# Kernel optimization log

Hardware: AMD Instinct MI355X
Metric: run time of the kernel (lower is better)

Reference implementation:

```python
import jax, jax.numpy as jnp
import numpy as np

N = 100000
E = 1600000
NEG_SLOPE = 0.2


def _param(key, shape, scale=0.05):
    return jax.random.normal(key, shape, dtype=jnp.float32) * scale


def setup_inputs() -> dict:
    key = jax.random.key(0)
    ks = jax.random.split(key, 16)
    x = jax.random.normal(ks[0], (N, 128), dtype=jnp.float32)
    edge_index = jax.random.randint(ks[1], (2, E), 0, N, dtype=jnp.int64)
    # layer 1: 128 -> (H=2, C=64), concat
    W1 = _param(ks[2], (128, 2 * 64)); a_src1 = _param(ks[3], (2, 64)); a_dst1 = _param(ks[4], (2, 64)); b1 = jnp.zeros((128,), jnp.float32)
    # layer 2: 128 -> (H=2, C=64), concat
    W2 = _param(ks[5], (128, 2 * 64)); a_src2 = _param(ks[6], (2, 64)); a_dst2 = _param(ks[7], (2, 64)); b2 = jnp.zeros((128,), jnp.float32)
    # layer 3: 128 -> (H=1, C=64), mean (concat=False)
    W3 = _param(ks[8], (128, 1 * 64)); a_src3 = _param(ks[9], (1, 64)); a_dst3 = _param(ks[10], (1, 64)); b3 = jnp.zeros((64,), jnp.float32)
    return {"x": x, "edge_index": edge_index,
            "W1": W1, "a_src1": a_src1, "a_dst1": a_dst1, "b1": b1,
            "W2": W2, "a_src2": a_src2, "a_dst2": a_dst2, "b2": b2,
            "W3": W3, "a_src3": a_src3, "a_dst3": a_dst3, "b3": b3}


def gat_layer(x, src, dst, W, a_src, a_dst, b, concat):
    H, C = a_src.shape
    n = x.shape[0]
    h = (x @ W).reshape(n, H, C)                      # [N,H,C]
    # per-node attention logits (avoid [E,H,C] gather for the score step)
    al_s = jnp.sum(h * a_src[None], axis=-1)          # [N,H]
    al_d = jnp.sum(h * a_dst[None], axis=-1)          # [N,H]
    e = al_s[src] + al_d[dst]                         # [E',H]
    e = jnp.where(e > 0, e, NEG_SLOPE * e)            # LeakyReLU(0.2)
    # scatter-softmax over incoming edges per destination node
    m = jax.ops.segment_max(e, dst, num_segments=n)   # [N,H]
    ex = jnp.exp(e - m[dst])
    z = jax.ops.segment_sum(ex, dst, num_segments=n)  # [N,H]
    alpha = ex / z[dst]                               # [E',H]
    msg = h[src] * alpha[:, :, None]                  # [E',H,C]
    out = jax.ops.segment_sum(msg, dst, num_segments=n)  # [N,H,C]
    out = out.reshape(n, H * C) if concat else out.mean(axis=1)
    return out + b


def reference(x, edge_index, W1, a_src1, a_dst1, b1, W2, a_src2, a_dst2, b2, W3, a_src3, a_dst3, b3):
    n = x.shape[0]
    loop = jnp.arange(n, dtype=edge_index.dtype)
    src = jnp.concatenate([edge_index[0], loop])      # add self-loops (PyG default)
    dst = jnp.concatenate([edge_index[1], loop])
    h = gat_layer(x, src, dst, W1, a_src1, a_dst1, b1, True)
    h = jax.nn.relu(h)
    h = gat_layer(h, src, dst, W2, a_src2, a_dst2, b2, True)
    h = jax.nn.relu(h)
    return gat_layer(h, src, dst, W3, a_src3, a_dst3, b3, False)
```

## Files before the change

kernel.cpp:

```cpp
#include <hip/hip_runtime.h>
#include <hip/hip_bf16.h>

#define NEG_SLOPE 0.2f
#define BUK_SHIFT 9
#define BUK_SIZE 512
#define BUK_CAP 16384

typedef unsigned short u16;
typedef __attribute__((ext_vector_type(4))) float f4v;
typedef _Float16 h8 __attribute__((ext_vector_type(8)));

__device__ __forceinline__ u16 f2h_bits(_Float16 h) {
    union { _Float16 f; u16 u; } c;
    c.f = h;
    return c.u;
}


__global__ void k_zero(int* g_cnt, int nb) {
    int i = blockIdx.x * blockDim.x + threadIdx.x;
    if (i < nb) g_cnt[i] = 0;
}

__launch_bounds__(256)
__global__ void k_binscatter(const int* __restrict__ ei, int* g_cnt, int* buckets,
                             int E, int nb) {
    __shared__ int lcnt[256], lbase[256], lcur[256];
    int t = threadIdx.x;
    if (t < nb) {
        lcnt[t] = 0;
        lcur[t] = 0;
    }
    __syncthreads();
    int tile0 = blockIdx.x * 4096;
    int pk[16], bk[16];
#pragma unroll
    for (int k = 0; k < 16; k++) {
        int idx = tile0 + k * 256 + t;
        bk[k] = -1;
        if (idx < E) {
            int s = ei[idx];
            int d = ei[E + idx];
            bk[k] = d >> BUK_SHIFT;
            pk[k] = (s << BUK_SHIFT) | (d & (BUK_SIZE - 1));
            atomicAdd(&lcnt[bk[k]], 1);
        }
    }
    __syncthreads();
    if (t < nb && lcnt[t] > 0) lbase[t] = atomicAdd(&g_cnt[t], lcnt[t]);
    __syncthreads();
#pragma unroll
    for (int k = 0; k < 16; k++) {
        if (bk[k] >= 0) {
            int p = lbase[bk[k]] + atomicAdd(&lcur[bk[k]], 1);
            if (p < BUK_CAP) buckets[(bk[k] << 14) + p] = pk[k];
        }
    }
}

__launch_bounds__(512)
__global__ void k_csr(const int* __restrict__ g_cnt, const int* __restrict__ buckets,
                      int* csr_ptr, int* csr_src, int n, int nb) {
    __shared__ int lcnt[512], lsc[512], lcur[512], bsc[512];
    int b = blockIdx.x;
    int t = threadIdx.x;
    int nodes = min(BUK_SIZE, n - b * BUK_SIZE);
    int cnt = min(g_cnt[b], BUK_CAP);
    const int* bp = &buckets[b << 14];

    int bv = 0;
    if (t < nb) bv = min(g_cnt[t], BUK_CAP) + min(BUK_SIZE, n - t * BUK_SIZE);
    bsc[t] = bv;
    __syncthreads();
    for (int off = 1; off < 512; off <<= 1) {
        int x = (t >= off) ? bsc[t - off] : 0;
        __syncthreads();
        bsc[t] += x;
        __syncthreads();
    }
    int boff = bsc[b] - (cnt + nodes);
    int total = bsc[nb - 1];
    __syncthreads();

    lcnt[t] = 0;
    __syncthreads();
    for (int i = t; i < cnt; i += 512) atomicAdd(&lcnt[bp[i] & (BUK_SIZE - 1)], 1);
    __syncthreads();
    int myc = (t < nodes) ? (lcnt[t] + 1) : 0;
    lsc[t] = myc;
    __syncthreads();
    for (int off = 1; off < 512; off <<= 1) {
        int x = (t >= off) ? lsc[t - off] : 0;
        __syncthreads();
        lsc[t] += x;
        __syncthreads();
    }
    int excl = lsc[t] - myc;
    lcur[t] = excl;
    if (t < nodes) csr_ptr[b * BUK_SIZE + t] = boff + excl;
    if (b == nb - 1 && t == 0) csr_ptr[n] = total;
    __syncthreads();
    for (int i = t; i < cnt; i += 512) {
        int v = bp[i];
        int ld = v & (BUK_SIZE - 1);
        int p = atomicAdd(&lcur[ld], 1);
        csr_src[boff + p] = v >> BUK_SHIFT;
    }
    if (t < nodes) {
        int p = atomicAdd(&lcur[t], 1);
        csr_src[boff + p] = b * BUK_SIZE + t;
    }
}


__global__ void k_wsplit_all(const float* __restrict__ W1, const float* __restrict__ W2,
                             const float* __restrict__ W3, u16* __restrict__ T1h,
                             u16* __restrict__ T1l, u16* __restrict__ T2h,
                             u16* __restrict__ T2l, u16* __restrict__ T3h,
                             u16* __restrict__ T3l) {
    int t = blockIdx.x * 256 + threadIdx.x;
    const float* W;
    u16 *Th, *Tl;
    int M, idx;
    if (t < 16384) {
        W = W1; Th = T1h; Tl = T1l; M = 128; idx = t;
    } else if (t < 32768) {
        W = W2; Th = T2h; Tl = T2l; M = 128; idx = t - 16384;
    } else if (t < 40960) {
        W = W3; Th = T3h; Tl = T3l; M = 64; idx = t - 32768;
    } else {
        return;
    }
    int c = idx >> 7, k = idx & 127;
    float v = W[(size_t)k * M + c];
    _Float16 h = (_Float16)v;
    _Float16 l = (_Float16)(v - (float)h);
    int ct = c >> 4, ch = k >> 5, q = (k >> 3) & 3, j = k & 7;
    size_t addr = ((size_t)ct * 4 + ch) * 512 + ((c & 15) + 16 * q) * 8 + j;
    Th[addr] = f2h_bits(h);
    Tl[addr] = f2h_bits(l);
}


__device__ __forceinline__ void load_split_f32(const float* __restrict__ X, int row,
                                               int koff, int N, h8& hi, h8& lo) {
    float v[8];
    if (row < N) {
        float4 a = *(const float4*)&X[(size_t)row * 128 + koff];
        float4 b = *(const float4*)&X[(size_t)row * 128 + koff + 4];
        v[0] = a.x; v[1] = a.y; v[2] = a.z; v[3] = a.w;
        v[4] = b.x; v[5] = b.y; v[6] = b.z; v[7] = b.w;
    } else {
#pragma unroll
        for (int i = 0; i < 8; i++) v[i] = 0.f;
    }
    union { h8 s; _Float16 u[8]; } H, L;
#pragma unroll
    for (int i = 0; i < 8; i++) {
        H.u[i] = (_Float16)v[i];
        L.u[i] = (_Float16)(v[i] - (float)H.u[i]);
    }
    hi = H.s;
    lo = L.s;
}

template <int M, bool FP32X>
__launch_bounds__(256)
__global__ void k_gemm_mfma(const float* __restrict__ Xf, const u16* __restrict__ XH,
                            const u16* __restrict__ WTh, const u16* __restrict__ WTl,
                            const float* __restrict__ asrc, const float* __restrict__ adst,
                            _Float16* __restrict__ Hout, float* __restrict__ als,
                            float* __restrict__ ald, int nrows) {
    const int CT = M / 16;
    const int H = (M == 128) ? 2 : 1;
    int tid = threadIdx.x;
    int wv = tid >> 6, lane = tid & 63;
    int q = lane >> 4, nl = lane & 15;
    int R0 = blockIdx.x * 128 + wv * 32;
    int rt0 = R0 >> 4;

    f4v acc[2][CT];
    f4v z4 = {0.f, 0.f, 0.f, 0.f};
#pragma unroll
    for (int rt = 0; rt < 2; rt++)
#pragma unroll
        for (int ct = 0; ct < CT; ct++) acc[rt][ct] = z4;

#pragma unroll
    for (int ch = 0; ch < 4; ch++) {
        h8 ah0, al0, ah1, al1;
        if (FP32X) {
            int koff = ch * 32 + q * 8;
            load_split_f32(Xf, R0 + nl, koff, nrows, ah0, al0);
            load_split_f32(Xf, R0 + 16 + nl, koff, nrows, ah1, al1);
        } else {
            size_t a0 = ((size_t)rt0 * 4 + ch) * 512 + lane * 8;
            size_t a1 = ((size_t)(rt0 + 1) * 4 + ch) * 512 + lane * 8;
            ah0 = *(const h8*)&XH[a0];
            ah1 = *(const h8*)&XH[a1];
        }
#pragma unroll
        for (int ct = 0; ct < CT; ct++) {
            size_t bb = ((size_t)ct * 4 + ch) * 512 + lane * 8;
            h8 bh = *(const h8*)&WTh[bb];
            h8 bl = *(const h8*)&WTl[bb];
            acc[0][ct] = __builtin_amdgcn_mfma_f32_16x16x32_f16(ah0, bh, acc[0][ct], 0, 0, 0);
            acc[0][ct] = __builtin_amdgcn_mfma_f32_16x16x32_f16(ah0, bl, acc[0][ct], 0, 0, 0);
            acc[1][ct] = __builtin_amdgcn_mfma_f32_16x16x32_f16(ah1, bh, acc[1][ct], 0, 0, 0);
            acc[1][ct] = __builtin_amdgcn_mfma_f32_16x16x32_f16(ah1, bl, acc[1][ct], 0, 0, 0);
            if (FP32X) {
                acc[0][ct] = __builtin_amdgcn_mfma_f32_16x16x32_f16(al0, bh, acc[0][ct], 0, 0, 0);
                acc[1][ct] = __builtin_amdgcn_mfma_f32_16x16x32_f16(al1, bh, acc[1][ct], 0, 0, 0);
            }
        }
    }

    float av[CT], dvv[CT];
#pragma unroll
    for (int ct = 0; ct < CT; ct++) {
        av[ct] = asrc[ct * 16 + nl];
        dvv[ct] = adst[ct * 16 + nl];
    }
    float ps[2][4][2], pd[2][4][2];
#pragma unroll
    for (int rt = 0; rt < 2; rt++)
#pragma unroll
        for (int r = 0; r < 4; r++)
            for (int h = 0; h < 2; h++) ps[rt][r][h] = pd[rt][r][h] = 0.f;
#pragma unroll
    for (int rt = 0; rt < 2; rt++)
#pragma unroll
        for (int ct = 0; ct < CT; ct++) {
            int h = (M == 128) ? (ct >> 2) : 0;
#pragma unroll
            for (int r = 0; r < 4; r++) {
                ps[rt][r][h] = fmaf(acc[rt][ct][r], av[ct], ps[rt][r][h]);
                pd[rt][r][h] = fmaf(acc[rt][ct][r], dvv[ct], pd[rt][r][h]);
            }
        }

#pragma unroll
    for (int rt = 0; rt < 2; rt++)
#pragma unroll
        for (int ct = 0; ct < CT; ct++)
#pragma unroll
            for (int r = 0; r < 4; r++) {
                int row = R0 + rt * 16 + q * 4 + r;
                if (row < nrows) Hout[(size_t)row * M + ct * 16 + nl] = (_Float16)acc[rt][ct][r];
            }

#pragma unroll
    for (int rt = 0; rt < 2; rt++)
#pragma unroll
        for (int r = 0; r < 4; r++)
#pragma unroll
            for (int h = 0; h < H; h++) {
                float v1 = ps[rt][r][h], v2 = pd[rt][r][h];
                for (int m = 1; m <= 8; m <<= 1) {
                    v1 += __shfl_xor(v1, m);
                    v2 += __shfl_xor(v2, m);
                }
                int row = R0 + rt * 16 + q * 4 + r;
                if (nl == 0 && row < nrows) {
                    als[(size_t)row * H + h] = v1;
                    ald[(size_t)row * H + h] = v2;
                }
            }
}


__launch_bounds__(256)
__global__ void k_agg128(const int* __restrict__ ptr, const int* __restrict__ srcv,
                         const _Float16* __restrict__ Hh, const float* __restrict__ als,
                         const float* __restrict__ ald, const float* __restrict__ bias,
                         u16* __restrict__ OutX, int n) {
    int wid = (blockIdx.x * blockDim.x + threadIdx.x) >> 6;
    int lane = threadIdx.x & 63;
    if (wid >= n) return;
    int start = ptr[wid], end = ptr[wid + 1];
    float2 adv = *(const float2*)&ald[(size_t)wid * 2];
    int grp = lane >> 4;
    int gl = lane & 15;
    int hsel = gl >> 3;
    float z0 = 0.f, z1 = 0.f;
    float acc[8];
#pragma unroll
    for (int c = 0; c < 8; c++) acc[c] = 0.f;

    for (int base = start; base < end; base += 64) {
        int i = base + lane;
        int s_l = 0;
        float ex0 = 0.f, ex1 = 0.f;
        if (i < end) {
            s_l = srcv[i];
            float2 av = *(const float2*)&als[(size_t)s_l * 2];
            float e0 = av.x + adv.x;
            e0 = e0 > 0.f ? e0 : NEG_SLOPE * e0;
            ex0 = __expf(e0);
            float e1 = av.y + adv.y;
            e1 = e1 > 0.f ? e1 : NEG_SLOPE * e1;
            ex1 = __expf(e1);
        }
        z0 += ex0;
        z1 += ex1;
        int cntj = min(64, end - base);
        for (int jp = 0; jp < cntj; jp += 32) {
            int nk = min(8, (cntj - jp + 3) >> 2);
            h8 hv[8];
            float w[8];
#pragma unroll
            for (int k = 0; k < 8; k++) {
                if (k < nk) {
                    int j = jp + 4 * k + grp;
                    int s = __shfl(s_l, j);
                    float w0 = __shfl(ex0, j);
                    float w1 = __shfl(ex1, j);
                    w[k] = hsel ? w1 : w0;
                    hv[k] = *(const h8*)&Hh[(size_t)s * 128 + gl * 8];
                }
            }
#pragma unroll
            for (int k = 0; k < 8; k++) {
                if (k < nk) {
#pragma unroll
                    for (int c = 0; c < 8; c++)
                        acc[c] = fmaf(w[k], (float)hv[k][c], acc[c]);
                }
            }
        }
    }

#pragma unroll
    for (int c = 0; c < 8; c++) {
        acc[c] += __shfl_xor(acc[c], 16);
        acc[c] += __shfl_xor(acc[c], 32);
    }
    for (int m = 32; m >= 1; m >>= 1) {
        z0 += __shfl_xor(z0, m);
        z1 += __shfl_xor(z1, m);
    }
    if (lane < 16) {
        float zinv = hsel ? (1.f / z1) : (1.f / z0);
        int c0 = gl * 8;
        float4 b0 = *(const float4*)&bias[c0];
        float4 b1 = *(const float4*)&bias[c0 + 4];
        float bb[8] = {b0.x, b0.y, b0.z, b0.w, b1.x, b1.y, b1.z, b1.w};
        union { _Float16 f[8]; h8 v; } O;
#pragma unroll
        for (int c = 0; c < 8; c++) {
            float o = fmaxf(fmaf(acc[c], zinv, bb[c]), 0.f);
            O.f[c] = (_Float16)o;
        }
        int ch = c0 >> 5, qq = (c0 >> 3) & 3;
        size_t tb = ((size_t)(wid >> 4) * 4 + ch) * 512 + ((size_t)((wid & 15) + 16 * qq)) * 8;
        *(h8*)&OutX[tb] = O.v;
    }
}


__launch_bounds__(256)
__global__ void k_agg64(const int* __restrict__ ptr, const int* __restrict__ srcv,
                        const _Float16* __restrict__ Hh, const float* __restrict__ als,
                        const float* __restrict__ ald, const float* __restrict__ bias,
                        float* __restrict__ Out, int n) {
    int wid = blockIdx.x * 4 + (threadIdx.x >> 6);
    int lane = threadIdx.x & 63;
    if (wid >= n) return;
    int start = ptr[wid], end = ptr[wid + 1];
    float ad0 = ald[wid];
    int grp = lane >> 3;
    int gl = lane & 7;
    float z = 0.f;
    float acc[8];
#pragma unroll
    for (int c = 0; c < 8; c++) acc[c] = 0.f;

    for (int base = start; base < end; base += 64) {
        int i = base + lane;
        int s_l = 0;
        float ex0 = 0.f;
        if (i < end) {
            s_l = srcv[i];
            float e = als[s_l] + ad0;
            e = e > 0.f ? e : NEG_SLOPE * e;
            ex0 = __expf(e);
        }
        z += ex0;
        int cntj = min(64, end - base);
        int nk = (cntj + 7) >> 3;
        h8 hv[8];
        float w[8];
#pragma unroll
        for (int k = 0; k < 8; k++) {
            if (k < nk) {
                int j = 8 * k + grp;
                int s = __shfl(s_l, j);
                w[k] = __shfl(ex0, j);
                hv[k] = *(const h8*)&Hh[(size_t)s * 64 + gl * 8];
            }
        }
#pragma unroll
        for (int k = 0; k < 8; k++) {
            if (k < nk) {
#pragma unroll
                for (int c = 0; c < 8; c++)
                    acc[c] = fmaf(w[k], (float)hv[k][c], acc[c]);
            }
        }
    }

#pragma unroll
    for (int c = 0; c < 8; c++) {
        acc[c] += __shfl_xor(acc[c], 8);
        acc[c] += __shfl_xor(acc[c], 16);
        acc[c] += __shfl_xor(acc[c], 32);
    }
    for (int m = 32; m >= 1; m >>= 1) z += __shfl_xor(z, m);
    if (lane < 8) {
        float zinv = 1.f / z;
        int c0 = gl * 8;
        float4 b0 = *(const float4*)&bias[c0];
        float4 b1 = *(const float4*)&bias[c0 + 4];
        float4 o1, o2;
        o1.x = fmaf(acc[0], zinv, b0.x);
        o1.y = fmaf(acc[1], zinv, b0.y);
        o1.z = fmaf(acc[2], zinv, b0.z);
        o1.w = fmaf(acc[3], zinv, b0.w);
        o2.x = fmaf(acc[4], zinv, b1.x);
        o2.y = fmaf(acc[5], zinv, b1.y);
        o2.z = fmaf(acc[6], zinv, b1.z);
        o2.w = fmaf(acc[7], zinv, b1.w);
        *(float4*)&Out[(size_t)wid * 64 + c0] = o1;
        *(float4*)&Out[(size_t)wid * 64 + c0 + 4] = o2;
    }
}


extern "C" void kernel_launch(void* const* d_in, const int* in_sizes, int n_in,
                              void* d_out, int out_size, void* d_ws, size_t ws_size,
                              hipStream_t stream) {
    const float* x = (const float*)d_in[0];
    const int* ei = (const int*)d_in[1];
    const float* W1 = (const float*)d_in[2];
    const float* as1 = (const float*)d_in[3];
    const float* ad1 = (const float*)d_in[4];
    const float* b1 = (const float*)d_in[5];
    const float* W2 = (const float*)d_in[6];
    const float* as2 = (const float*)d_in[7];
    const float* ad2 = (const float*)d_in[8];
    const float* b2 = (const float*)d_in[9];
    const float* W3 = (const float*)d_in[10];
    const float* as3 = (const float*)d_in[11];
    const float* ad3 = (const float*)d_in[12];
    const float* b3 = (const float*)d_in[13];

    const int N = in_sizes[0] / 128;
    const int E = in_sizes[1] / 2;
    const int NB = (N + BUK_SIZE - 1) / BUK_SIZE;
    const int Npad = (N + 127) & ~127;

    char* p = (char*)d_ws;
    auto alloc = [&](size_t bytes) -> char* {
        char* r = p;
        p += (bytes + 255) & ~(size_t)255;
        return r;
    };
    int* g_cnt = (int*)alloc(256 * 4);
    int* buckets = (int*)alloc((size_t)NB * BUK_CAP * 4);
    int* csr_ptr = (int*)alloc((size_t)(N + 1) * 4);
    int* csr_src = (int*)alloc((size_t)(E + N) * 4);
    float* als = (float*)alloc((size_t)N * 2 * 4);
    float* aldv = (float*)alloc((size_t)N * 2 * 4);
    _Float16* Hbuf = (_Float16*)alloc((size_t)N * 128 * 2);
    u16* XH = (u16*)alloc((size_t)Npad * 128 * 2);
    u16* WT1h = (u16*)alloc(128 * 128 * 2);
    u16* WT1l = (u16*)alloc(128 * 128 * 2);
    u16* WT2h = (u16*)alloc(128 * 128 * 2);
    u16* WT2l = (u16*)alloc(128 * 128 * 2);
    u16* WT3h = (u16*)alloc(128 * 64 * 2);
    u16* WT3l = (u16*)alloc(128 * 64 * 2);

    const int nbG = Npad / 128;
    const int nbWave = (N * 64 + 255) / 256;
    const int nbAgg64 = (N + 3) / 4;
    const int nbTile = (E + 4095) / 4096;

    k_zero<<<1, 256, 0, stream>>>(g_cnt, 256);
    k_binscatter<<<nbTile, 256, 0, stream>>>(ei, g_cnt, buckets, E, NB);
    k_csr<<<NB, 512, 0, stream>>>(g_cnt, buckets, csr_ptr, csr_src, N, NB);

    k_wsplit_all<<<160, 256, 0, stream>>>(W1, W2, W3, WT1h, WT1l, WT2h, WT2l, WT3h, WT3l);

    k_gemm_mfma<128, true><<<nbG, 256, 0, stream>>>(x, nullptr, WT1h, WT1l,
                                                    as1, ad1, Hbuf, als, aldv, N);
    k_agg128<<<nbWave, 256, 0, stream>>>(csr_ptr, csr_src, Hbuf, als, aldv, b1, XH, N);

    k_gemm_mfma<128, false><<<nbG, 256, 0, stream>>>(nullptr, XH, WT2h, WT2l,
                                                     as2, ad2, Hbuf, als, aldv, N);
    k_agg128<<<nbWave, 256, 0, stream>>>(csr_ptr, csr_src, Hbuf, als, aldv, b2, XH, N);

    k_gemm_mfma<64, false><<<nbG, 256, 0, stream>>>(nullptr, XH, WT3h, WT3l,
                                                    as3, ad3, Hbuf, als, aldv, N);
    k_agg64<<<nbAgg64, 256, 0, stream>>>(csr_ptr, csr_src, Hbuf, als, aldv, b3,
                                         (float*)d_out, N);
}
```

Measured before the change: 453.3 us.

## Process multiple destination nodes per wavefront in GAT aggregation kernels

The aggregation kernels now give each wavefront 4 destination nodes (128-wide layers) or 8 nodes (64-wide layer) instead of one. Each node gets a 16- or 8-lane group, and the loop runs to the max degree within the wave. This removes the cross-lane accumulator reductions and the idle lanes seen with average degree around 17. It adds divergence when degrees differ inside a wave. The separate zeroing kernel is also folded into the weight-split kernel to drop a launch.

```diff
diff --git a/kernel.cpp b/kernel.cpp
--- a/kernel.cpp
+++ b/kernel.cpp
@@ -16,11 +16,6 @@
     return c.u;
 }
 
-
-__global__ void k_zero(int* g_cnt, int nb) {
-    int i = blockIdx.x * blockDim.x + threadIdx.x;
-    if (i < nb) g_cnt[i] = 0;
-}
 
 __launch_bounds__(256)
 __global__ void k_binscatter(const int* __restrict__ ei, int* g_cnt, int* buckets,
@@ -117,8 +112,9 @@
                              const float* __restrict__ W3, u16* __restrict__ T1h,
                              u16* __restrict__ T1l, u16* __restrict__ T2h,
                              u16* __restrict__ T2l, u16* __restrict__ T3h,
-                             u16* __restrict__ T3l) {
+                             u16* __restrict__ T3l, int* __restrict__ g_cnt) {
     int t = blockIdx.x * 256 + threadIdx.x;
+    if (t < 256) g_cnt[t] = 0;
     const float* W;
     u16 *Th, *Tl;
     int M, idx;
@@ -274,25 +270,32 @@
                          const _Float16* __restrict__ Hh, const float* __restrict__ als,
                          const float* __restrict__ ald, const float* __restrict__ bias,
                          u16* __restrict__ OutX, int n) {
-    int wid = (blockIdx.x * blockDim.x + threadIdx.x) >> 6;
+    int wvg = (blockIdx.x * blockDim.x + threadIdx.x) >> 6;
     int lane = threadIdx.x & 63;
-    if (wid >= n) return;
-    int start = ptr[wid], end = ptr[wid + 1];
-    float2 adv = *(const float2*)&ald[(size_t)wid * 2];
-    int grp = lane >> 4;
+    int nn = lane >> 4;
     int gl = lane & 15;
+    int wid = wvg * 4 + nn;
+    bool valid = wid < n;
+    int widc = valid ? wid : (n - 1);
+    int start = ptr[widc];
+    int deg = valid ? (ptr[widc + 1] - start) : 0;
+    int md = deg;
+    md = max(md, __shfl_xor(md, 16));
+    md = max(md, __shfl_xor(md, 32));
+    float2 adv = *(const float2*)&ald[(size_t)widc * 2];
     int hsel = gl >> 3;
+    int coff = gl * 8;
     float z0 = 0.f, z1 = 0.f;
     float acc[8];
 #pragma unroll
     for (int c = 0; c < 8; c++) acc[c] = 0.f;
 
-    for (int base = start; base < end; base += 64) {
-        int i = base + lane;
+    for (int base = 0; base < md; base += 16) {
+        int i = base + gl;
         int s_l = 0;
         float ex0 = 0.f, ex1 = 0.f;
-        if (i < end) {
-            s_l = srcv[i];
+        if (i < deg) {
+            s_l = srcv[start + i];
             float2 av = *(const float2*)&als[(size_t)s_l * 2];
             float e0 = av.x + adv.x;
             e0 = e0 > 0.f ? e0 : NEG_SLOPE * e0;
@@ -303,24 +306,24 @@
         }
         z0 += ex0;
         z1 += ex1;
-        int cntj = min(64, end - base);
-        for (int jp = 0; jp < cntj; jp += 32) {
-            int nk = min(8, (cntj - jp + 3) >> 2);
-            h8 hv[8];
-            float w[8];
-#pragma unroll
-            for (int k = 0; k < 8; k++) {
+        int cnt = min(16, md - base);
+        for (int jp = 0; jp < cnt; jp += 4) {
+            int nk = min(4, cnt - jp);
+            h8 hv[4];
+            float w[4];
+#pragma unroll
+            for (int k = 0; k < 4; k++) {
                 if (k < nk) {
-                    int j = jp + 4 * k + grp;
+                    int j = nn * 16 + jp + k;
                     int s = __shfl(s_l, j);
                     float w0 = __shfl(ex0, j);
                     float w1 = __shfl(ex1, j);
                     w[k] = hsel ? w1 : w0;
-                    hv[k] = *(const h8*)&Hh[(size_t)s * 128 + gl * 8];
+                    hv[k] = *(const h8*)&Hh[(size_t)s * 128 + coff];
                 }
             }
 #pragma unroll
-            for (int k = 0; k < 8; k++) {
+            for (int k = 0; k < 4; k++) {
                 if (k < nk) {
 #pragma unroll
                     for (int c = 0; c < 8; c++)
@@ -331,19 +334,14 @@
     }
 
 #pragma unroll
-    for (int c = 0; c < 8; c++) {
-        acc[c] += __shfl_xor(acc[c], 16);
-        acc[c] += __shfl_xor(acc[c], 32);
-    }
-    for (int m = 32; m >= 1; m >>= 1) {
+    for (int m = 1; m <= 8; m <<= 1) {
         z0 += __shfl_xor(z0, m);
         z1 += __shfl_xor(z1, m);
     }
-    if (lane < 16) {
+    if (valid) {
         float zinv = hsel ? (1.f / z1) : (1.f / z0);
-        int c0 = gl * 8;
-        float4 b0 = *(const float4*)&bias[c0];
-        float4 b1 = *(const float4*)&bias[c0 + 4];
+        float4 b0 = *(const float4*)&bias[coff];
+        float4 b1 = *(const float4*)&bias[coff + 4];
         float bb[8] = {b0.x, b0.y, b0.z, b0.w, b1.x, b1.y, b1.z, b1.w};
         union { _Float16 f[8]; h8 v; } O;
 #pragma unroll
@@ -351,7 +349,7 @@
             float o = fmaxf(fmaf(acc[c], zinv, bb[c]), 0.f);
             O.f[c] = (_Float16)o;
         }
-        int ch = c0 >> 5, qq = (c0 >> 3) & 3;
+        int ch = coff >> 5, qq = (coff >> 3) & 3;
         size_t tb = ((size_t)(wid >> 4) * 4 + ch) * 512 + ((size_t)((wid & 15) + 16 * qq)) * 8;
         *(h8*)&OutX[tb] = O.v;
     }
@@ -363,64 +361,68 @@
                         const _Float16* __restrict__ Hh, const float* __restrict__ als,
                         const float* __restrict__ ald, const float* __restrict__ bias,
                         float* __restrict__ Out, int n) {
-    int wid = blockIdx.x * 4 + (threadIdx.x >> 6);
+    int wvg = (blockIdx.x * blockDim.x + threadIdx.x) >> 6;
     int lane = threadIdx.x & 63;
-    if (wid >= n) return;
-    int start = ptr[wid], end = ptr[wid + 1];
-    float ad0 = ald[wid];
-    int grp = lane >> 3;
+    int nn = lane >> 3;
     int gl = lane & 7;
+    int wid = wvg * 8 + nn;
+    bool valid = wid < n;
+    int widc = valid ? wid : (n - 1);
+    int start = ptr[widc];
+    int deg = valid ? (ptr[widc + 1] - start) : 0;
+    int md = deg;
+    md = max(md, __shfl_xor(md, 8));
+    md = max(md, __shfl_xor(md, 16));
+    md = max(md, __shfl_xor(md, 32));
+    float ad0 = ald[widc];
+    int coff = gl * 8;
     float z = 0.f;
     float acc[8];
 #pragma unroll
     for (int c = 0; c < 8; c++) acc[c] = 0.f;
 
-    for (int base = start; base < end; base += 64) {
-        int i = base + lane;
+    for (int base = 0; base < md; base += 8) {
+        int i = base + gl;
         int s_l = 0;
         float ex0 = 0.f;
-        if (i < end) {
-            s_l = srcv[i];
+        if (i < deg) {
+            s_l = srcv[start + i];
             float e = als[s_l] + ad0;
             e = e > 0.f ? e : NEG_SLOPE * e;
             ex0 = __expf(e);
         }
         z += ex0;
-        int cntj = min(64, end - base);
-        int nk = (cntj + 7) >> 3;
-        h8 hv[8];
-        float w[8];
-#pragma unroll
-        for (int k = 0; k < 8; k++) {
-            if (k < nk) {
-                int j = 8 * k + grp;
-                int s = __shfl(s_l, j);
-                w[k] = __shfl(ex0, j);
-                hv[k] = *(const h8*)&Hh[(size_t)s * 64 + gl * 8];
-            }
-        }
-#pragma unroll
-        for (int k = 0; k < 8; k++) {
-            if (k < nk) {
-#pragma unroll
-                for (int c = 0; c < 8; c++)
-                    acc[c] = fmaf(w[k], (float)hv[k][c], acc[c]);
-            }
-        }
-    }
-
-#pragma unroll
-    for (int c = 0; c < 8; c++) {
-        acc[c] += __shfl_xor(acc[c], 8);
-        acc[c] += __shfl_xor(acc[c], 16);
-        acc[c] += __shfl_xor(acc[c], 32);
-    }
-    for (int m = 32; m >= 1; m >>= 1) z += __shfl_xor(z, m);
-    if (lane < 8) {
+        int cnt = min(8, md - base);
+        for (int jp = 0; jp < cnt; jp += 4) {
+            int nk = min(4, cnt - jp);
+            h8 hv[4];
+            float w[4];
+#pragma unroll
+            for (int k = 0; k < 4; k++) {
+                if (k < nk) {
+                    int j = nn * 8 + jp + k;
+                    int s = __shfl(s_l, j);
+                    w[k] = __shfl(ex0, j);
+                    hv[k] = *(const h8*)&Hh[(size_t)s * 64 + coff];
+                }
+            }
+#pragma unroll
+            for (int k = 0; k < 4; k++) {
+                if (k < nk) {
+#pragma unroll
+                    for (int c = 0; c < 8; c++)
+                        acc[c] = fmaf(w[k], (float)hv[k][c], acc[c]);
+                }
+            }
+        }
+    }
+
+#pragma unroll
+    for (int m = 1; m <= 4; m <<= 1) z += __shfl_xor(z, m);
+    if (valid) {
         float zinv = 1.f / z;
-        int c0 = gl * 8;
-        float4 b0 = *(const float4*)&bias[c0];
-        float4 b1 = *(const float4*)&bias[c0 + 4];
+        float4 b0 = *(const float4*)&bias[coff];
+        float4 b1 = *(const float4*)&bias[coff + 4];
         float4 o1, o2;
         o1.x = fmaf(acc[0], zinv, b0.x);
         o1.y = fmaf(acc[1], zinv, b0.y);
@@ -430,8 +432,8 @@
         o2.y = fmaf(acc[5], zinv, b1.y);
         o2.z = fmaf(acc[6], zinv, b1.z);
         o2.w = fmaf(acc[7], zinv, b1.w);
-        *(float4*)&Out[(size_t)wid * 64 + c0] = o1;
-        *(float4*)&Out[(size_t)wid * 64 + c0 + 4] = o2;
+        *(float4*)&Out[(size_t)wid * 64 + coff] = o1;
+        *(float4*)&Out[(size_t)wid * 64 + coff + 4] = o2;
     }
 }
 
@@ -481,23 +483,25 @@
     u16* WT3l = (u16*)alloc(128 * 64 * 2);
 
     const int nbG = Npad / 128;
-    const int nbWave = (N * 64 + 255) / 256;
-    const int nbAgg64 = (N + 3) / 4;
+    const int waves128 = (N + 3) / 4;
+    const int nbAgg128 = (waves128 + 3) / 4;
+    const int waves64 = (N + 7) / 8;
+    const int nbAgg64 = (waves64 + 3) / 4;
     const int nbTile = (E + 4095) / 4096;
 
-    k_zero<<<1, 256, 0, stream>>>(g_cnt, 256);
+    k_wsplit_all<<<160, 256, 0, stream>>>(W1, W2, W3, WT1h, WT1l, WT2h, WT2l, WT3h,
+                                          WT3l, g_cnt);
+
     k_binscatter<<<nbTile, 256, 0, stream>>>(ei, g_cnt, buckets, E, NB);
     k_csr<<<NB, 512, 0, stream>>>(g_cnt, buckets, csr_ptr, csr_src, N, NB);
 
-    k_wsplit_all<<<160, 256, 0, stream>>>(W1, W2, W3, WT1h, WT1l, WT2h, WT2l, WT3h, WT3l);
-
     k_gemm_mfma<128, true><<<nbG, 256, 0, stream>>>(x, nullptr, WT1h, WT1l,
                                                     as1, ad1, Hbuf, als, aldv, N);
-    k_agg128<<<nbWave, 256, 0, stream>>>(csr_ptr, csr_src, Hbuf, als, aldv, b1, XH, N);
+    k_agg128<<<nbAgg128, 256, 0, stream>>>(csr_ptr, csr_src, Hbuf, als, aldv, b1, XH, N);
 
     k_gemm_mfma<128, false><<<nbG, 256, 0, stream>>>(nullptr, XH, WT2h, WT2l,
                                                      as2, ad2, Hbuf, als, aldv, N);
-    k_agg128<<<nbWave, 256, 0, stream>>>(csr_ptr, csr_src, Hbuf, als, aldv, b2, XH, N);
+    k_agg128<<<nbAgg128, 256, 0, stream>>>(csr_ptr, csr_src, Hbuf, als, aldv, b2, XH, N);
 
     k_gemm_mfma<64, false><<<nbG, 256, 0, stream>>>(nullptr, XH, WT3h, WT3l,
                                                     as3, ad3, Hbuf, als, aldv, N);
```

Measured after the change: 418.8 us. 1.08x faster.
